# Kernel tuning notes

Hardware: AMD Instinct MI355X
Metric: run time of the kernel (lower is better)

Reference implementation:

```python
import jax, jax.numpy as jnp
import numpy as np

N_QUBITS = 12
N_LAYERS = 4
BATCH = 4096
DIM = 2 ** N_QUBITS


def _ry(t):
    # t: (B,) real -> (B,2,2) complex64 ; RY = [[c,-s],[s,c]], c=cos(t/2), s=sin(t/2)
    c = jnp.cos(t / 2).astype(jnp.complex64)
    s = jnp.sin(t / 2).astype(jnp.complex64)
    return jnp.stack([jnp.stack([c, -s], -1), jnp.stack([s, c], -1)], -2)


def _rx(t):
    # RX = [[c,-i s],[-i s,c]]
    c = jnp.cos(t / 2).astype(jnp.complex64)
    s = (-1j) * jnp.sin(t / 2).astype(jnp.complex64)
    return jnp.stack([jnp.stack([c, s], -1), jnp.stack([s, c], -1)], -2)


def _rz(t):
    # RZ = diag(e^{-i t/2}, e^{+i t/2})
    e = jnp.exp(-0.5j * t.astype(jnp.complex64))
    z = jnp.zeros_like(e)
    return jnp.stack([jnp.stack([e, z], -1), jnp.stack([z, jnp.conj(e)], -1)], -2)


def _apply1(state, q, mat):
    # state: (B, 2^n) complex; mat: (B,2,2); qubit q is the q-th most significant bit
    B = state.shape[0]
    s = state.reshape(B, 2 ** q, 2, -1)
    return jnp.einsum('bij,bajm->baim', mat, s).reshape(B, DIM)


_CNOT_PERM = np.array([0, 1, 3, 2])  # control=1 -> flip target


def _cnot_adj(state, c):
    # CNOT(control=c, target=c+1), adjacent qubits
    B = state.shape[0]
    s = state.reshape(B, 2 ** c, 4, -1)
    return s[:, :, _CNOT_PERM, :].reshape(B, DIM)


def _parity():
    idx = np.arange(DIM)
    pop = np.zeros(DIM, dtype=np.int64)
    for k in range(N_QUBITS):
        pop += (idx >> k) & 1
    return jnp.asarray(1.0 - 2.0 * (pop % 2), dtype=jnp.float32)


def setup_inputs() -> dict:
    key = jax.random.key(0)
    k1, k2 = jax.random.split(key)
    x = jax.random.uniform(k1, (BATCH,), dtype=jnp.float32)
    thetas = jax.random.normal(k2, (N_LAYERS, N_QUBITS, 3), dtype=jnp.float32)
    return {"x": x, "thetas": thetas}


def reference(x, thetas):
    x = x.ravel()
    B = x.shape[0]
    x1 = jnp.arcsin(x)          # RY feature-map angles
    x2 = jnp.arccos(x ** 2)     # RZ feature-map angles
    state = jnp.zeros((B, DIM), jnp.complex64).at[:, 0].set(1.0)
    ry_fm = _ry(x1)
    rz_fm = _rz(x2)
    for l in range(N_LAYERS):
        for q in range(N_QUBITS):
            state = _apply1(state, q, ry_fm)
        for q in range(N_QUBITS):
            state = _apply1(state, q, rz_fm)
        for q in range(N_QUBITS):
            t = thetas[l, q]
            state = _apply1(state, q, _rx(jnp.broadcast_to(t[0], (B,))))
            state = _apply1(state, q, _rz(jnp.broadcast_to(t[1], (B,))))
            state = _apply1(state, q, _rx(jnp.broadcast_to(t[2], (B,))))
        for j in range(N_QUBITS - 1):
            state = _cnot_adj(state, j)
    abs2 = jnp.real(state) ** 2 + jnp.imag(state) ** 2
    return jnp.einsum('bs,s->b', abs2, _parity())  # <Z0 Z1 ... Z_{n-1}> per batch
```

## Files before the change

kernel.cpp:

```cpp
#include <hip/hip_runtime.h>

namespace {

constexpr int NQ = 12;
constexpr int DIM = 1 << NQ;
constexpr int THREADS = 256;

struct c32 { float r, i; };

__device__ __forceinline__ c32 cmul(c32 a, c32 b) {
    return { fmaf(a.r, b.r, -(a.i * b.i)), fmaf(a.r, b.i, a.i * b.r) };
}

__device__ __forceinline__ void bfy(c32& x, c32& y, float cb, float sb) {
    const c32 a = x, b = y;
    x.r = fmaf(cb, a.r, -(sb * b.r));
    x.i = fmaf(cb, a.i, -(sb * b.i));
    y.r = fmaf(sb, a.r, cb * b.r);
    y.i = fmaf(sb, a.i, cb * b.i);
}

template<int BP>
__device__ __forceinline__ void applyRY(c32 v[16], float cb, float sb) {
    #pragma unroll
    for (int mi = 0; mi < 8; ++mi) {
        const int i0 = ((mi >> BP) << (BP + 1)) | (mi & ((1 << BP) - 1));
        bfy(v[i0], v[i0 | (1 << BP)], cb, sb);
    }
}

__host__ __device__ constexpr int G(int t, int k) {
    for (int i = 0; i < k; ++i) t = (t ^ (t >> 1)) & 0xFFF;
    return t;
}
__host__ __device__ constexpr int Cm(int t) {
    int lo = 0;
    if (t & 0x010) lo ^= 0x2;
    if (t & 0x020) lo ^= 0x4;
    if (t & 0x040) lo ^= 0x8;
    if (t & 0x080) lo ^= 0x6;
    if (t & 0x100) lo ^= 0xA;
    if (t & 0x200) lo ^= 0xC;
    return t ^ lo;
}

__device__ __forceinline__ void diagTree(c32 T[16], c32 C,
                                         const c32 pf0[4], const c32 pf1[4],
                                         const c32 qv[4], int sigma) {
    const c32 one = { 1.f, 0.f };
    T[0] = C;
    #pragma unroll
    for (int m = 3; m >= 0; --m) {
        const c32 qs0 = sigma ? qv[m] : one;
        const c32 qs1 = sigma ? one : qv[m];
        const c32 g00 = cmul(pf0[m], qs0);
        const c32 g01 = cmul(pf0[m], qs1);
        const c32 g10 = cmul(pf1[m], qs0);
        const c32 g11 = cmul(pf1[m], qs1);
        #pragma unroll
        for (int e = (1 << (3 - m)) - 1; e >= 0; --e) {
            const int j0 = e << (m + 1);
            const int sfxhi = __popc(e) & 1;
            const c32 ga = sfxhi ? g01 : g00;
            const c32 gb = sfxhi ? g10 : g11;
            T[j0 | (1 << m)] = cmul(T[j0], gb);
            T[j0]            = cmul(T[j0], ga);
        }
    }
}

__global__ __launch_bounds__(THREADS)
void qcirc_kernel(const float* __restrict__ x, const float* __restrict__ thetas,
                  float* __restrict__ out) {
    __shared__ alignas(16) float2 amp[DIM];
    __shared__ float4 Vs[4 * NQ * 2];
    __shared__ float2 TbS[2][2][16];
    __shared__ float2 CHiS[2][16];
    __shared__ float2 CLoS[2][2][16];
    __shared__ float red[4];
    float4* a4 = reinterpret_cast<float4*>(amp);

    const int tid = threadIdx.x;
    const int b = blockIdx.x;

    const float xv = x[b];
    const float x1 = asinf(xv);
    const float x2 = acosf(xv * xv);
    const float cy = cosf(0.5f * x1), sy = sinf(0.5f * x1);
    const float cz = cosf(0.5f * x2), sz = sinf(0.5f * x2);
    const c32 M00 = {  cz * cy, -sz * cy };
    const c32 M01 = { -cz * sy,  sz * sy };
    const c32 M10 = {  cz * sy,  sz * sy };
    const c32 M11 = {  cz * cy,  sz * cy };

    if (tid < 4 * NQ) {
        const float* th = thetas + tid * 3;
        const float h0 = 0.5f * th[0], h1 = 0.5f * th[1], h2 = 0.5f * th[2];
        const float c0 = cosf(h0), s0 = sinf(h0);
        const float c1 = cosf(h1), s1 = sinf(h1);
        const float c2 = cosf(h2), s2 = sinf(h2);
        const c32 z0 = { c1, -s1 }, z1 = { c1, s1 };
        const c32 X00 = { c0, 0.f }, X01 = { 0.f, -s0 };
        const c32 A00 = cmul(z0, X00), A01 = cmul(z0, X01);
        const c32 A10 = cmul(z1, X01), A11 = cmul(z1, X00);
        const c32 Y00 = { c2, 0.f }, Y01 = { 0.f, -s2 };
        const c32 U00 = { Y00.r*A00.r - Y00.i*A00.i + Y01.r*A10.r - Y01.i*A10.i,
                          Y00.r*A00.i + Y00.i*A00.r + Y01.r*A10.i + Y01.i*A10.r };
        const c32 U01 = { Y00.r*A01.r - Y00.i*A01.i + Y01.r*A11.r - Y01.i*A11.i,
                          Y00.r*A01.i + Y00.i*A01.r + Y01.r*A11.i + Y01.i*A11.r };
        const c32 U10 = { Y01.r*A00.r - Y01.i*A00.i + Y00.r*A10.r - Y00.i*A10.i,
                          Y01.r*A00.i + Y01.i*A00.r + Y00.r*A10.i + Y00.i*A10.r };
        const c32 U11 = { Y01.r*A01.r - Y01.i*A01.i + Y00.r*A11.r - Y00.i*A11.i,
                          Y01.r*A01.i + Y01.i*A01.r + Y00.r*A11.i + Y00.i*A11.r };
        const c32 V00 = { U00.r*M00.r - U00.i*M00.i + U01.r*M10.r - U01.i*M10.i,
                          U00.r*M00.i + U00.i*M00.r + U01.r*M10.i + U01.i*M10.r };
        const c32 V01 = { U00.r*M01.r - U00.i*M01.i + U01.r*M11.r - U01.i*M11.i,
                          U00.r*M01.i + U00.i*M01.r + U01.r*M11.i + U01.i*M11.r };
        const c32 V10 = { U10.r*M00.r - U10.i*M00.i + U11.r*M10.r - U11.i*M10.i,
                          U10.r*M00.i + U10.i*M00.r + U11.r*M10.i + U11.i*M10.r };
        const c32 V11 = { U10.r*M01.r - U10.i*M01.i + U11.r*M11.r - U11.i*M11.i,
                          U10.r*M01.i + U10.i*M01.r + U11.r*M11.i + U11.i*M11.r };

        float cb = sqrtf(V00.r*V00.r + V00.i*V00.i);
        float sb = sqrtf(V10.r*V10.r + V10.i*V10.i);
        c32 p0, p1, q1;
        const float eps = 1e-6f;
        if (sb <= eps) {
            const float icb = 1.f / cb;
            p0 = { V00.r*icb, V00.i*icb };
            p1 = { V11.r*icb, V11.i*icb };
            q1 = { 1.f, 0.f };
            cb = 1.f; sb = 0.f;
        } else if (cb <= eps) {
            const float isb = 1.f / sb;
            p1 = { V10.r*isb, V10.i*isb };
            p0 = { -V01.r*isb, -V01.i*isb };
            q1 = { 1.f, 0.f };
            cb = 0.f; sb = 1.f;
        } else {
            const float icb = 1.f / cb, isb = 1.f / sb;
            p0 = { V00.r*icb, V00.i*icb };
            p1 = { V10.r*isb, V10.i*isb };
            const c32 t = { V11.r*p1.r + V11.i*p1.i, V11.i*p1.r - V11.r*p1.i };
            q1 = { t.r*icb, t.i*icb };
        }
        Vs[tid * 2]     = make_float4(cb, sb, p0.r, p0.i);
        Vs[tid * 2 + 1] = make_float4(p1.r, p1.i, q1.r, q1.i);
    }
    __syncthreads();

    if (tid < 64) {
        const int bK = (tid >> 5) + 1;
        const int sg = (tid >> 4) & 1;
        const int j  = tid & 15;
        c32 acc = { 1.f, 0.f };
        #pragma unroll
        for (int m = 3; m >= 0; --m) {
            const int Q = 11 - m;
            const float4 s0 = Vs[(bK*NQ+Q)*2];
            const float4 s1 = Vs[(bK*NQ+Q)*2+1];
            const float4 n1 = Vs[((bK+1)*NQ+Q)*2+1];
            const c32 pf = ((j >> m) & 1) ? c32{ s1.x, s1.y } : c32{ s0.z, s0.w };
            acc = cmul(acc, pf);
            if (sg ^ (__popc(j >> m) & 1)) acc = cmul(acc, c32{ n1.z, n1.w });
        }
        TbS[bK-1][sg][j] = make_float2(acc.r, acc.i);
    } else if (tid < 96) {
        const int idx = tid - 64;
        const int bK = (idx >> 4) + 1;
        const int h  = idx & 15;
        c32 acc = { 1.f, 0.f };
        #pragma unroll
        for (int Q = 0; Q < 4; ++Q) {
            const float4 s0 = Vs[(bK*NQ+Q)*2];
            const float4 s1 = Vs[(bK*NQ+Q)*2+1];
            const float4 n1 = Vs[((bK+1)*NQ+Q)*2+1];
            const c32 pf = ((h >> (3-Q)) & 1) ? c32{ s1.x, s1.y } : c32{ s0.z, s0.w };
            acc = cmul(acc, pf);
            if (__popc(h >> (3-Q)) & 1) acc = cmul(acc, c32{ n1.z, n1.w });
        }
        CHiS[bK-1][h] = make_float2(acc.r, acc.i);
    } else if (tid < 160) {
        const int idx = tid - 96;
        const int bK = (idx >> 5) + 1;
        const int sh = (idx >> 4) & 1;
        const int lo = idx & 15;
        c32 acc = { 1.f, 0.f };
        #pragma unroll
        for (int Q = 4; Q < 8; ++Q) {
            const float4 s0 = Vs[(bK*NQ+Q)*2];
            const float4 s1 = Vs[(bK*NQ+Q)*2+1];
            const float4 n1 = Vs[((bK+1)*NQ+Q)*2+1];
            const c32 pf = ((lo >> (7-Q)) & 1) ? c32{ s1.x, s1.y } : c32{ s0.z, s0.w };
            acc = cmul(acc, pf);
            if (sh ^ (__popc(lo >> (7-Q)) & 1)) acc = cmul(acc, c32{ n1.z, n1.w });
        }
        CLoS[bK-1][sh][lo] = make_float2(acc.r, acc.i);
    }

    {
        const int sg0 = __popc(tid) & 1;
        c32 C = { 1.f, 0.f };
        #pragma unroll
        for (int q = 0; q < 8; ++q) {
            const float4 s0 = Vs[q*2];
            const float4 s1 = Vs[q*2+1];
            const bool bit = (tid >> (7 - q)) & 1;
            const c32 e = bit ? c32{ s1.x * s0.y, s1.y * s0.y }
                             : c32{ s0.z * s0.x, s0.w * s0.x };
            C = cmul(C, e);
            const float4 n1 = Vs[(NQ+q)*2+1];
            if (__popc(tid >> (7 - q)) & 1) C = cmul(C, c32{ n1.z, n1.w });
        }
        c32 pf0[4], pf1[4], qv[4];
        #pragma unroll
        for (int m = 0; m < 4; ++m) {
            const int Q = 11 - m;
            const float4 s0 = Vs[Q*2];
            const float4 s1 = Vs[Q*2+1];
            const float4 n1 = Vs[(NQ+Q)*2+1];
            pf0[m] = { s0.z * s0.x, s0.w * s0.x };
            pf1[m] = { s1.x * s0.y, s1.y * s0.y };
            qv[m]  = { n1.z, n1.w };
        }
        c32 T[16];
        diagTree(T, C, pf0, pf1, qv, sg0);
        const int beta = Cm(tid << 4);
        #pragma unroll
        for (int m = 0; m < 8; ++m)
            a4[(beta ^ (2 * m)) >> 1] =
                make_float4(T[2*m].r, T[2*m].i, T[2*m+1].r, T[2*m+1].i);
    }
    __syncthreads();

    const int Lo = tid & 15, Hh = tid >> 4;
    float acc = 0.f;

    #define RUN_LAYER(K)                                                            \
    {                                                                               \
                                              \
        {                                                                           \
            const float4 g0 = Vs[(K*NQ+0)*2], g1 = Vs[(K*NQ+1)*2];                  \
            const float4 g2 = Vs[(K*NQ+2)*2], g3 = Vs[(K*NQ+3)*2];                  \
            const int beta = Cm(G(tid, K));                                         \
            c32 v[16];                                                              \
            _Pragma("unroll")                                                       \
            for (int j = 0; j < 16; ++j) {                                          \
                const float2 t = amp[beta ^ Cm(G(j << 8, K))];                      \
                v[j] = { t.x, t.y };                                                \
            }                                                                       \
            applyRY<3>(v, g0.x, g0.y); applyRY<2>(v, g1.x, g1.y);                   \
            applyRY<1>(v, g2.x, g2.y); applyRY<0>(v, g3.x, g3.y);                   \
            _Pragma("unroll")                                                       \
            for (int j = 0; j < 16; ++j)                                            \
                amp[beta ^ Cm(G(j << 8, K))] = make_float2(v[j].r, v[j].i);         \
            __syncthreads();                                                        \
        }                                                                           \
                                               \
        {                                                                           \
            const float4 g0 = Vs[(K*NQ+4)*2], g1 = Vs[(K*NQ+5)*2];                  \
            const float4 g2 = Vs[(K*NQ+6)*2], g3 = Vs[(K*NQ+7)*2];                  \
            const int beta = Cm(G((Hh << 8) | Lo, K));                              \
            c32 v[16];                                                              \
            _Pragma("unroll")                                                       \
            for (int j = 0; j < 16; ++j) {                                          \
                const float2 t = amp[beta ^ Cm(G(j << 4, K))];                      \
                v[j] = { t.x, t.y };                                                \
            }                                                                       \
            applyRY<3>(v, g0.x, g0.y); applyRY<2>(v, g1.x, g1.y);                   \
            applyRY<1>(v, g2.x, g2.y); applyRY<0>(v, g3.x, g3.y);                   \
            _Pragma("unroll")                                                       \
            for (int j = 0; j < 16; ++j)                                            \
                amp[beta ^ Cm(G(j << 4, K))] = make_float2(v[j].r, v[j].i);         \
            __syncthreads();                                                        \
        }                                                                           \
                                  \
        {                                                                           \
            const float4 g0 = Vs[(K*NQ+8)*2],  g1 = Vs[(K*NQ+9)*2];                 \
            const float4 g2 = Vs[(K*NQ+10)*2], g3 = Vs[(K*NQ+11)*2];                \
            const int beta = Cm(G((Hh << 8) | (Lo << 4), K));                       \
            c32 v[16];                                                              \
            _Pragma("unroll")                                                       \
            for (int m = 0; m < 8; ++m) {                                           \
                const int gg = Cm(G(2 * m, K));                                     \
                const float4 F = a4[(beta ^ (gg & ~1)) >> 1];                       \
                const c32 flo = { F.x, F.y }, fhi = { F.z, F.w };                   \
                if (gg & 1) { v[2*m+1] = flo; v[2*m] = fhi; }                       \
                else        { v[2*m] = flo;   v[2*m+1] = fhi; }                     \
            }                                                                       \
            applyRY<3>(v, g0.x, g0.y); applyRY<2>(v, g1.x, g1.y);                   \
            applyRY<1>(v, g2.x, g2.y); applyRY<0>(v, g3.x, g3.y);                   \
            if constexpr (K < 3) {                                                  \
                const int sgm = __popc(tid) & 1;                                    \
                const int sgh = __popc(tid >> 4) & 1;                               \
                const float2 ch = CHiS[K-1][Hh];                                    \
                const float2 cl = CLoS[K-1][sgh][Lo];                               \
                const c32 CT = cmul(c32{ch.x,ch.y}, c32{cl.x,cl.y});                \
                _Pragma("unroll")                                                   \
                for (int j = 0; j < 16; ++j) {                                      \
                    const float2 tb = TbS[K-1][sgm][j];                             \
                    v[j] = cmul(v[j], cmul(CT, c32{tb.x, tb.y}));                   \
                }                                                                   \
                _Pragma("unroll")                                                   \
                for (int m = 0; m < 8; ++m) {                                       \
                    const int gg = Cm(G(2 * m, K));                                 \
                    float4 F;                                                       \
                    if (gg & 1) F = make_float4(v[2*m+1].r, v[2*m+1].i, v[2*m].r,   v[2*m].i); \
                    else        F = make_float4(v[2*m].r,   v[2*m].i,   v[2*m+1].r, v[2*m+1].i); \
                    a4[(beta ^ (gg & ~1)) >> 1] = F;                                \
                }                                                                   \
                __syncthreads();                                                    \
            } else {                                                                \
                 \
                const int sgnHL = (__popc(Hh & 5) ^ __popc(Lo & 5)) & 1;            \
                _Pragma("unroll")                                                   \
                for (int j = 0; j < 16; ++j) {                                      \
                    const float m2 = fmaf(v[j].r, v[j].r, v[j].i * v[j].i);         \
                    acc += ((sgnHL ^ __popc(j & 5)) & 1) ? -m2 : m2;                \
                }                                                                   \
            }                                                                       \
        }                                                                           \
    }

    RUN_LAYER(1)
    RUN_LAYER(2)
    RUN_LAYER(3)
    #undef RUN_LAYER

    #pragma unroll
    for (int off = 32; off > 0; off >>= 1) acc += __shfl_down(acc, off, 64);
    if ((tid & 63) == 0) red[tid >> 6] = acc;
    __syncthreads();
    if (tid == 0) out[b] = red[0] + red[1] + red[2] + red[3];
}

}

extern "C" void kernel_launch(void* const* d_in, const int* in_sizes, int n_in,
                              void* d_out, int out_size, void* d_ws, size_t ws_size,
                              hipStream_t stream) {
    const float* x      = (const float*)d_in[0];
    const float* thetas = (const float*)d_in[1];
    float* out          = (float*)d_out;
    const int batch = in_sizes[0];
    qcirc_kernel<<<batch, THREADS, 0, stream>>>(x, thetas, out);
}
```

Baseline: 90.75 us.

## Process two batch elements per block with interleaved float4 shared-memory state

Each block now simulates two batch elements at once, storing both statevectors interleaved as float4 in shared memory so every shared load and store moves two amplitudes. Per-block setup, table construction and barriers are shared across the pair, and the launch uses half as many blocks with launch_bounds hinting two blocks per CU. The cost is doubled register pressure per thread (two 16-element complex arrays) and 64 KB of shared memory per block, which may limit occupancy. The grid assumes an even batch size.

```diff
diff --git a/kernel.cpp b/kernel.cpp
--- a/kernel.cpp
+++ b/kernel.cpp
@@ -3,7 +3,6 @@
 namespace {
 
 constexpr int NQ = 12;
-constexpr int DIM = 1 << NQ;
 constexpr int THREADS = 256;
 
 struct c32 { float r, i; };
@@ -69,32 +68,33 @@
     }
 }
 
-__global__ __launch_bounds__(THREADS)
+__global__ __launch_bounds__(THREADS, 2)
 void qcirc_kernel(const float* __restrict__ x, const float* __restrict__ thetas,
                   float* __restrict__ out) {
-    __shared__ alignas(16) float2 amp[DIM];
-    __shared__ float4 Vs[4 * NQ * 2];
-    __shared__ float2 TbS[2][2][16];
-    __shared__ float2 CHiS[2][16];
-    __shared__ float2 CLoS[2][2][16];
-    __shared__ float red[4];
-    float4* a4 = reinterpret_cast<float4*>(amp);
+    __shared__ alignas(16) float4 amp4[4096];
+    __shared__ float4 Vs[2][96];
+    __shared__ float2 TbS[2][2][2][16];
+    __shared__ float2 CHiS[2][2][16];
+    __shared__ float2 CLoS[2][2][2][16];
+    __shared__ float red[2][4];
 
     const int tid = threadIdx.x;
-    const int b = blockIdx.x;
-
-    const float xv = x[b];
-    const float x1 = asinf(xv);
-    const float x2 = acosf(xv * xv);
-    const float cy = cosf(0.5f * x1), sy = sinf(0.5f * x1);
-    const float cz = cosf(0.5f * x2), sz = sinf(0.5f * x2);
-    const c32 M00 = {  cz * cy, -sz * cy };
-    const c32 M01 = { -cz * sy,  sz * sy };
-    const c32 M10 = {  cz * sy,  sz * sy };
-    const c32 M11 = {  cz * cy,  sz * cy };
-
-    if (tid < 4 * NQ) {
-        const float* th = thetas + tid * 3;
+    const int blk = blockIdx.x;
+
+    if (tid < 96) {
+        const int e = tid >= 48;
+        const int g = tid - 48 * e;
+        const float xv = x[2 * blk + e];
+        const float x1 = asinf(xv);
+        const float x2 = acosf(xv * xv);
+        const float cy = cosf(0.5f * x1), sy = sinf(0.5f * x1);
+        const float cz = cosf(0.5f * x2), sz = sinf(0.5f * x2);
+        const c32 M00 = {  cz * cy, -sz * cy };
+        const c32 M01 = { -cz * sy,  sz * sy };
+        const c32 M10 = {  cz * sy,  sz * sy };
+        const c32 M11 = {  cz * cy,  sz * cy };
+
+        const float* th = thetas + g * 3;
         const float h0 = 0.5f * th[0], h1 = 0.5f * th[1], h2 = 0.5f * th[2];
         const float c0 = cosf(h0), s0 = sinf(h0);
         const float c1 = cosf(h1), s1 = sinf(h1);
@@ -144,194 +144,206 @@
             const c32 t = { V11.r*p1.r + V11.i*p1.i, V11.i*p1.r - V11.r*p1.i };
             q1 = { t.r*icb, t.i*icb };
         }
-        Vs[tid * 2]     = make_float4(cb, sb, p0.r, p0.i);
-        Vs[tid * 2 + 1] = make_float4(p1.r, p1.i, q1.r, q1.i);
+        Vs[e][g * 2]     = make_float4(cb, sb, p0.r, p0.i);
+        Vs[e][g * 2 + 1] = make_float4(p1.r, p1.i, q1.r, q1.i);
     }
     __syncthreads();
 
-    if (tid < 64) {
-        const int bK = (tid >> 5) + 1;
-        const int sg = (tid >> 4) & 1;
-        const int j  = tid & 15;
-        c32 acc = { 1.f, 0.f };
-        #pragma unroll
-        for (int m = 3; m >= 0; --m) {
-            const int Q = 11 - m;
-            const float4 s0 = Vs[(bK*NQ+Q)*2];
-            const float4 s1 = Vs[(bK*NQ+Q)*2+1];
-            const float4 n1 = Vs[((bK+1)*NQ+Q)*2+1];
-            const c32 pf = ((j >> m) & 1) ? c32{ s1.x, s1.y } : c32{ s0.z, s0.w };
-            acc = cmul(acc, pf);
-            if (sg ^ (__popc(j >> m) & 1)) acc = cmul(acc, c32{ n1.z, n1.w });
-        }
-        TbS[bK-1][sg][j] = make_float2(acc.r, acc.i);
-    } else if (tid < 96) {
-        const int idx = tid - 64;
-        const int bK = (idx >> 4) + 1;
-        const int h  = idx & 15;
-        c32 acc = { 1.f, 0.f };
-        #pragma unroll
-        for (int Q = 0; Q < 4; ++Q) {
-            const float4 s0 = Vs[(bK*NQ+Q)*2];
-            const float4 s1 = Vs[(bK*NQ+Q)*2+1];
-            const float4 n1 = Vs[((bK+1)*NQ+Q)*2+1];
-            const c32 pf = ((h >> (3-Q)) & 1) ? c32{ s1.x, s1.y } : c32{ s0.z, s0.w };
-            acc = cmul(acc, pf);
-            if (__popc(h >> (3-Q)) & 1) acc = cmul(acc, c32{ n1.z, n1.w });
-        }
-        CHiS[bK-1][h] = make_float2(acc.r, acc.i);
-    } else if (tid < 160) {
-        const int idx = tid - 96;
-        const int bK = (idx >> 5) + 1;
-        const int sh = (idx >> 4) & 1;
-        const int lo = idx & 15;
-        c32 acc = { 1.f, 0.f };
-        #pragma unroll
-        for (int Q = 4; Q < 8; ++Q) {
-            const float4 s0 = Vs[(bK*NQ+Q)*2];
-            const float4 s1 = Vs[(bK*NQ+Q)*2+1];
-            const float4 n1 = Vs[((bK+1)*NQ+Q)*2+1];
-            const c32 pf = ((lo >> (7-Q)) & 1) ? c32{ s1.x, s1.y } : c32{ s0.z, s0.w };
-            acc = cmul(acc, pf);
-            if (sh ^ (__popc(lo >> (7-Q)) & 1)) acc = cmul(acc, c32{ n1.z, n1.w });
-        }
-        CLoS[bK-1][sh][lo] = make_float2(acc.r, acc.i);
-    }
+    #define BUILD_TABLES(E, VID)                                                     \
+    {                                                                                \
+        const int vid = (VID);                                                       \
+        if (vid < 64) {                                                              \
+            const int bK = (vid >> 5) + 1;                                           \
+            const int sg = (vid >> 4) & 1;                                           \
+            const int j  = vid & 15;                                                 \
+            c32 acc = { 1.f, 0.f };                                                  \
+            _Pragma("unroll")                                                        \
+            for (int m = 3; m >= 0; --m) {                                           \
+                const int Q = 11 - m;                                                \
+                const float4 s0 = Vs[E][(bK*NQ+Q)*2];                                \
+                const float4 s1 = Vs[E][(bK*NQ+Q)*2+1];                              \
+                const float4 n1 = Vs[E][((bK+1)*NQ+Q)*2+1];                          \
+                const c32 pf = ((j >> m) & 1) ? c32{ s1.x, s1.y } : c32{ s0.z, s0.w }; \
+                acc = cmul(acc, pf);                                                 \
+                if (sg ^ (__popc(j >> m) & 1)) acc = cmul(acc, c32{ n1.z, n1.w });   \
+            }                                                                        \
+            TbS[E][bK-1][sg][j] = make_float2(acc.r, acc.i);                         \
+        } else if (vid < 96) {                                                       \
+            const int idx = vid - 64;                                               \
+            const int bK = (idx >> 4) + 1;                                           \
+            const int h  = idx & 15;                                                 \
+            c32 acc = { 1.f, 0.f };                                                  \
+            _Pragma("unroll")                                                        \
+            for (int Q = 0; Q < 4; ++Q) {                                            \
+                const float4 s0 = Vs[E][(bK*NQ+Q)*2];                                \
+                const float4 s1 = Vs[E][(bK*NQ+Q)*2+1];                              \
+                const float4 n1 = Vs[E][((bK+1)*NQ+Q)*2+1];                          \
+                const c32 pf = ((h >> (3-Q)) & 1) ? c32{ s1.x, s1.y } : c32{ s0.z, s0.w }; \
+                acc = cmul(acc, pf);                                                 \
+                if (__popc(h >> (3-Q)) & 1) acc = cmul(acc, c32{ n1.z, n1.w });      \
+            }                                                                        \
+            CHiS[E][bK-1][h] = make_float2(acc.r, acc.i);                            \
+        } else if (vid < 160) {                                                      \
+            const int idx = vid - 96;                                               \
+            const int bK = (idx >> 5) + 1;                                           \
+            const int sh = (idx >> 4) & 1;                                           \
+            const int lo = idx & 15;                                                 \
+            c32 acc = { 1.f, 0.f };                                                  \
+            _Pragma("unroll")                                                        \
+            for (int Q = 4; Q < 8; ++Q) {                                            \
+                const float4 s0 = Vs[E][(bK*NQ+Q)*2];                                \
+                const float4 s1 = Vs[E][(bK*NQ+Q)*2+1];                              \
+                const float4 n1 = Vs[E][((bK+1)*NQ+Q)*2+1];                          \
+                const c32 pf = ((lo >> (7-Q)) & 1) ? c32{ s1.x, s1.y } : c32{ s0.z, s0.w }; \
+                acc = cmul(acc, pf);                                                 \
+                if (sh ^ (__popc(lo >> (7-Q)) & 1)) acc = cmul(acc, c32{ n1.z, n1.w }); \
+            }                                                                        \
+            CLoS[E][bK-1][sh][lo] = make_float2(acc.r, acc.i);                       \
+        }                                                                            \
+    }
+
+    if (tid < 160) BUILD_TABLES(0, tid)
+    if (tid >= 96) BUILD_TABLES(1, tid - 96)
+    #undef BUILD_TABLES
 
     {
         const int sg0 = __popc(tid) & 1;
-        c32 C = { 1.f, 0.f };
+        c32 T0[16], T1[16];
         #pragma unroll
-        for (int q = 0; q < 8; ++q) {
-            const float4 s0 = Vs[q*2];
-            const float4 s1 = Vs[q*2+1];
-            const bool bit = (tid >> (7 - q)) & 1;
-            const c32 e = bit ? c32{ s1.x * s0.y, s1.y * s0.y }
-                             : c32{ s0.z * s0.x, s0.w * s0.x };
-            C = cmul(C, e);
-            const float4 n1 = Vs[(NQ+q)*2+1];
-            if (__popc(tid >> (7 - q)) & 1) C = cmul(C, c32{ n1.z, n1.w });
+        for (int e = 0; e < 2; ++e) {
+            c32 C = { 1.f, 0.f };
+            #pragma unroll
+            for (int q = 0; q < 8; ++q) {
+                const float4 s0 = Vs[e][q*2];
+                const float4 s1 = Vs[e][q*2+1];
+                const bool bit = (tid >> (7 - q)) & 1;
+                const c32 ee = bit ? c32{ s1.x * s0.y, s1.y * s0.y }
+                                  : c32{ s0.z * s0.x, s0.w * s0.x };
+                C = cmul(C, ee);
+                const float4 n1 = Vs[e][(NQ+q)*2+1];
+                if (__popc(tid >> (7 - q)) & 1) C = cmul(C, c32{ n1.z, n1.w });
+            }
+            c32 pf0[4], pf1[4], qv[4];
+            #pragma unroll
+            for (int m = 0; m < 4; ++m) {
+                const int Q = 11 - m;
+                const float4 s0 = Vs[e][Q*2];
+                const float4 s1 = Vs[e][Q*2+1];
+                const float4 n1 = Vs[e][(NQ+Q)*2+1];
+                pf0[m] = { s0.z * s0.x, s0.w * s0.x };
+                pf1[m] = { s1.x * s0.y, s1.y * s0.y };
+                qv[m]  = { n1.z, n1.w };
+            }
+            diagTree(e == 0 ? T0 : T1, C, pf0, pf1, qv, sg0);
         }
-        c32 pf0[4], pf1[4], qv[4];
-        #pragma unroll
-        for (int m = 0; m < 4; ++m) {
-            const int Q = 11 - m;
-            const float4 s0 = Vs[Q*2];
-            const float4 s1 = Vs[Q*2+1];
-            const float4 n1 = Vs[(NQ+Q)*2+1];
-            pf0[m] = { s0.z * s0.x, s0.w * s0.x };
-            pf1[m] = { s1.x * s0.y, s1.y * s0.y };
-            qv[m]  = { n1.z, n1.w };
-        }
-        c32 T[16];
-        diagTree(T, C, pf0, pf1, qv, sg0);
         const int beta = Cm(tid << 4);
         #pragma unroll
-        for (int m = 0; m < 8; ++m)
-            a4[(beta ^ (2 * m)) >> 1] =
-                make_float4(T[2*m].r, T[2*m].i, T[2*m+1].r, T[2*m+1].i);
+        for (int j = 0; j < 16; ++j)
+            amp4[beta ^ j] = make_float4(T0[j].r, T0[j].i, T1[j].r, T1[j].i);
     }
     __syncthreads();
 
     const int Lo = tid & 15, Hh = tid >> 4;
-    float acc = 0.f;
-
-    #define RUN_LAYER(K)                                                            \
-    {                                                                               \
-                                              \
-        {                                                                           \
-            const float4 g0 = Vs[(K*NQ+0)*2], g1 = Vs[(K*NQ+1)*2];                  \
-            const float4 g2 = Vs[(K*NQ+2)*2], g3 = Vs[(K*NQ+3)*2];                  \
-            const int beta = Cm(G(tid, K));                                         \
-            c32 v[16];                                                              \
-            _Pragma("unroll")                                                       \
-            for (int j = 0; j < 16; ++j) {                                          \
-                const float2 t = amp[beta ^ Cm(G(j << 8, K))];                      \
-                v[j] = { t.x, t.y };                                                \
-            }                                                                       \
-            applyRY<3>(v, g0.x, g0.y); applyRY<2>(v, g1.x, g1.y);                   \
-            applyRY<1>(v, g2.x, g2.y); applyRY<0>(v, g3.x, g3.y);                   \
-            _Pragma("unroll")                                                       \
-            for (int j = 0; j < 16; ++j)                                            \
-                amp[beta ^ Cm(G(j << 8, K))] = make_float2(v[j].r, v[j].i);         \
-            __syncthreads();                                                        \
-        }                                                                           \
-                                               \
-        {                                                                           \
-            const float4 g0 = Vs[(K*NQ+4)*2], g1 = Vs[(K*NQ+5)*2];                  \
-            const float4 g2 = Vs[(K*NQ+6)*2], g3 = Vs[(K*NQ+7)*2];                  \
-            const int beta = Cm(G((Hh << 8) | Lo, K));                              \
-            c32 v[16];                                                              \
-            _Pragma("unroll")                                                       \
-            for (int j = 0; j < 16; ++j) {                                          \
-                const float2 t = amp[beta ^ Cm(G(j << 4, K))];                      \
-                v[j] = { t.x, t.y };                                                \
-            }                                                                       \
-            applyRY<3>(v, g0.x, g0.y); applyRY<2>(v, g1.x, g1.y);                   \
-            applyRY<1>(v, g2.x, g2.y); applyRY<0>(v, g3.x, g3.y);                   \
-            _Pragma("unroll")                                                       \
-            for (int j = 0; j < 16; ++j)                                            \
-                amp[beta ^ Cm(G(j << 4, K))] = make_float2(v[j].r, v[j].i);         \
-            __syncthreads();                                                        \
-        }                                                                           \
-                                  \
-        {                                                                           \
-            const float4 g0 = Vs[(K*NQ+8)*2],  g1 = Vs[(K*NQ+9)*2];                 \
-            const float4 g2 = Vs[(K*NQ+10)*2], g3 = Vs[(K*NQ+11)*2];                \
-            const int beta = Cm(G((Hh << 8) | (Lo << 4), K));                       \
-            c32 v[16];                                                              \
-            _Pragma("unroll")                                                       \
-            for (int m = 0; m < 8; ++m) {                                           \
-                const int gg = Cm(G(2 * m, K));                                     \
-                const float4 F = a4[(beta ^ (gg & ~1)) >> 1];                       \
-                const c32 flo = { F.x, F.y }, fhi = { F.z, F.w };                   \
-                if (gg & 1) { v[2*m+1] = flo; v[2*m] = fhi; }                       \
-                else        { v[2*m] = flo;   v[2*m+1] = fhi; }                     \
-            }                                                                       \
-            applyRY<3>(v, g0.x, g0.y); applyRY<2>(v, g1.x, g1.y);                   \
-            applyRY<1>(v, g2.x, g2.y); applyRY<0>(v, g3.x, g3.y);                   \
-            if constexpr (K < 3) {                                                  \
-                const int sgm = __popc(tid) & 1;                                    \
-                const int sgh = __popc(tid >> 4) & 1;                               \
-                const float2 ch = CHiS[K-1][Hh];                                    \
-                const float2 cl = CLoS[K-1][sgh][Lo];                               \
-                const c32 CT = cmul(c32{ch.x,ch.y}, c32{cl.x,cl.y});                \
-                _Pragma("unroll")                                                   \
-                for (int j = 0; j < 16; ++j) {                                      \
-                    const float2 tb = TbS[K-1][sgm][j];                             \
-                    v[j] = cmul(v[j], cmul(CT, c32{tb.x, tb.y}));                   \
-                }                                                                   \
-                _Pragma("unroll")                                                   \
-                for (int m = 0; m < 8; ++m) {                                       \
-                    const int gg = Cm(G(2 * m, K));                                 \
-                    float4 F;                                                       \
-                    if (gg & 1) F = make_float4(v[2*m+1].r, v[2*m+1].i, v[2*m].r,   v[2*m].i); \
-                    else        F = make_float4(v[2*m].r,   v[2*m].i,   v[2*m+1].r, v[2*m+1].i); \
-                    a4[(beta ^ (gg & ~1)) >> 1] = F;                                \
-                }                                                                   \
-                __syncthreads();                                                    \
-            } else {                                                                \
-                 \
-                const int sgnHL = (__popc(Hh & 5) ^ __popc(Lo & 5)) & 1;            \
-                _Pragma("unroll")                                                   \
-                for (int j = 0; j < 16; ++j) {                                      \
-                    const float m2 = fmaf(v[j].r, v[j].r, v[j].i * v[j].i);         \
-                    acc += ((sgnHL ^ __popc(j & 5)) & 1) ? -m2 : m2;                \
-                }                                                                   \
-            }                                                                       \
-        }                                                                           \
-    }
-
-    RUN_LAYER(1)
-    RUN_LAYER(2)
-    RUN_LAYER(3)
-    #undef RUN_LAYER
+    float accA = 0.f, accB = 0.f;
+
+    #define PASS_CORE(K, SH, BASEEXPR, Q0)                                           \
+        const float4 A0 = Vs[0][((K)*NQ+(Q0))*2],   A1 = Vs[0][((K)*NQ+(Q0)+1)*2];   \
+        const float4 A2 = Vs[0][((K)*NQ+(Q0)+2)*2], A3 = Vs[0][((K)*NQ+(Q0)+3)*2];   \
+        const float4 B0 = Vs[1][((K)*NQ+(Q0))*2],   B1 = Vs[1][((K)*NQ+(Q0)+1)*2];   \
+        const float4 B2 = Vs[1][((K)*NQ+(Q0)+2)*2], B3 = Vs[1][((K)*NQ+(Q0)+3)*2];   \
+        const int base = Cm(G((BASEEXPR), (K)));                                     \
+        c32 vA[16], vB[16];                                                          \
+        _Pragma("unroll")                                                            \
+        for (int j = 0; j < 16; ++j) {                                               \
+            const float4 F = amp4[base ^ Cm(G(j << (SH), (K)))];                     \
+            vA[j] = { F.x, F.y }; vB[j] = { F.z, F.w };                              \
+        }                                                                            \
+        applyRY<3>(vA, A0.x, A0.y); applyRY<2>(vA, A1.x, A1.y);                      \
+        applyRY<1>(vA, A2.x, A2.y); applyRY<0>(vA, A3.x, A3.y);                      \
+        applyRY<3>(vB, B0.x, B0.y); applyRY<2>(vB, B1.x, B1.y);                      \
+        applyRY<1>(vB, B2.x, B2.y); applyRY<0>(vB, B3.x, B3.y);
+
+    #define PASS_STORE(K, SH)                                                        \
+        _Pragma("unroll")                                                            \
+        for (int j = 0; j < 16; ++j)                                                 \
+            amp4[base ^ Cm(G(j << (SH), (K)))] =                                     \
+                make_float4(vA[j].r, vA[j].i, vB[j].r, vB[j].i);                     \
+        __syncthreads();
+
+    #define RUN_PASS_PLAIN(K, SH, BASEEXPR, Q0)                                      \
+    {                                                                                \
+        PASS_CORE(K, SH, BASEEXPR, Q0)                                               \
+        PASS_STORE(K, SH)                                                            \
+    }
+
+    #define RUN_PASS_DIAG(K)                                                         \
+    {                                                                                \
+        PASS_CORE(K, 0, (Hh << 8) | (Lo << 4), 8)                                    \
+        const int sgm = __popc(tid) & 1;                                             \
+        const int sgh = __popc(tid >> 4) & 1;                                        \
+        {                                                                            \
+            const float2 ch = CHiS[0][K-1][Hh];                                      \
+            const float2 cl = CLoS[0][K-1][sgh][Lo];                                 \
+            const c32 CT = cmul(c32{ch.x,ch.y}, c32{cl.x,cl.y});                     \
+            _Pragma("unroll")                                                        \
+            for (int j = 0; j < 16; ++j) {                                           \
+                const float2 tb = TbS[0][K-1][sgm][j];                               \
+                vA[j] = cmul(vA[j], cmul(CT, c32{tb.x, tb.y}));                      \
+            }                                                                        \
+        }                                                                            \
+        {                                                                            \
+            const float2 ch = CHiS[1][K-1][Hh];                                      \
+            const float2 cl = CLoS[1][K-1][sgh][Lo];                                 \
+            const c32 CT = cmul(c32{ch.x,ch.y}, c32{cl.x,cl.y});                     \
+            _Pragma("unroll")                                                        \
+            for (int j = 0; j < 16; ++j) {                                           \
+                const float2 tb = TbS[1][K-1][sgm][j];                               \
+                vB[j] = cmul(vB[j], cmul(CT, c32{tb.x, tb.y}));                      \
+            }                                                                        \
+        }                                                                            \
+        PASS_STORE(K, 0)                                                             \
+    }
+
+    #define RUN_PASS_OUT(K)                                                          \
+    {                                                                                \
+        PASS_CORE(K, 0, (Hh << 8) | (Lo << 4), 8)                                    \
+        const int sgnHL = (__popc(Hh & 5) ^ __popc(Lo & 5)) & 1;                     \
+        _Pragma("unroll")                                                            \
+        for (int j = 0; j < 16; ++j) {                                               \
+            const float mA = fmaf(vA[j].r, vA[j].r, vA[j].i * vA[j].i);              \
+            const float mB = fmaf(vB[j].r, vB[j].r, vB[j].i * vB[j].i);              \
+            if ((sgnHL ^ __popc(j & 5)) & 1) { accA -= mA; accB -= mB; }             \
+            else                             { accA += mA; accB += mB; }             \
+        }                                                                            \
+    }
+
+    RUN_PASS_PLAIN(1, 8, tid, 0)
+    RUN_PASS_PLAIN(1, 4, (Hh << 8) | Lo, 4)
+    RUN_PASS_DIAG(1)
+    RUN_PASS_PLAIN(2, 8, tid, 0)
+    RUN_PASS_PLAIN(2, 4, (Hh << 8) | Lo, 4)
+    RUN_PASS_DIAG(2)
+    RUN_PASS_PLAIN(3, 8, tid, 0)
+    RUN_PASS_PLAIN(3, 4, (Hh << 8) | Lo, 4)
+    RUN_PASS_OUT(3)
+
+    #undef RUN_PASS_PLAIN
+    #undef RUN_PASS_DIAG
+    #undef RUN_PASS_OUT
+    #undef PASS_CORE
+    #undef PASS_STORE
 
     #pragma unroll
-    for (int off = 32; off > 0; off >>= 1) acc += __shfl_down(acc, off, 64);
-    if ((tid & 63) == 0) red[tid >> 6] = acc;
+    for (int off = 32; off > 0; off >>= 1) {
+        accA += __shfl_down(accA, off, 64);
+        accB += __shfl_down(accB, off, 64);
+    }
+    if ((tid & 63) == 0) { red[0][tid >> 6] = accA; red[1][tid >> 6] = accB; }
     __syncthreads();
-    if (tid == 0) out[b] = red[0] + red[1] + red[2] + red[3];
+    if (tid == 0) {
+        out[2 * blk]     = red[0][0] + red[0][1] + red[0][2] + red[0][3];
+        out[2 * blk + 1] = red[1][0] + red[1][1] + red[1][2] + red[1][3];
+    }
 }
 
 }
@@ -343,5 +355,5 @@
     const float* thetas = (const float*)d_in[1];
     float* out          = (float*)d_out;
     const int batch = in_sizes[0];
-    qcirc_kernel<<<batch, THREADS, 0, stream>>>(x, thetas, out);
-}
+    qcirc_kernel<<<batch / 2, THREADS, 0, stream>>>(x, thetas, out);
+}
```

After: 113.7 us. 1.25x slower.
